# Optimization experiments

Measured on AMD Instinct MI355X. Metric: run time of the kernel, lower is better.

Reference implementation:

```python
import math
import jax, jax.numpy as jnp
import numpy as np

NUM_HEADS = 32

def _alibi_slopes(n: int) -> jnp.ndarray:
    cp2 = 2 ** int(math.floor(math.log2(n)))
    base = 2.0 ** (-(2.0 ** (-(math.log2(cp2) - 3))))
    slopes = base ** np.arange(1, cp2 + 1, dtype=np.float64)
    if cp2 != n:
        extra_base = 2.0 ** (-(2.0 ** (-(math.log2(2 * cp2) - 3))))
        rem = min(cp2, n - cp2)
        slopes = np.concatenate([slopes, extra_base ** np.arange(1, 1 + 2 * rem, 2, dtype=np.float64)])
    return jnp.asarray(slopes, dtype=jnp.float32)


def setup_inputs() -> dict:
    key = jax.random.key(0)
    k1, k2, k3 = jax.random.split(key, 3)
    B, S, E, H, D = 2, 2048, 4096, NUM_HEADS, 128
    hidden_states = jax.random.normal(k1, (B, S, E), dtype=jnp.float32)
    # torch Linear y = x @ W^T; we store transposed weights [in, out]
    w_qkv = jax.random.normal(k2, (E, H * D + 2 * D), dtype=jnp.float32) * 0.02
    w_c = jax.random.normal(k3, (E, E), dtype=jnp.float32) * 0.02
    return {"hidden_states": hidden_states, "w_qkv": w_qkv, "w_c": w_c}


def reference(hidden_states, w_qkv, w_c):
    B, S, E = hidden_states.shape
    H = NUM_HEADS
    D = E // H
    scaling = D ** -0.5

    qkv = hidden_states @ w_qkv                      # [B,S,H*D+2D]
    q = qkv[..., : H * D].reshape(B, S, H, D)        # [B,S,H,D]
    k = qkv[..., H * D: H * D + D]                   # [B,S,D] single KV head (MQA)
    v = qkv[..., H * D + D:]                         # [B,S,D]

    pos = jnp.arange(S)
    slopes = _alibi_slopes(H)                        # [H]
    # ALiBi: slope * (k_pos - q_pos), <= 0 in the causal region
    bias = slopes[:, None, None] * (pos[None, None, :] - pos[None, :, None]).astype(jnp.float32)  # [H,S,S]

    scores = jnp.einsum('bqhd,bkd->bhqk', q, k) * scaling + bias[None]  # [B,H,S,S]
    causal = pos[:, None] >= pos[None, :]            # [S,S]
    scores = jnp.where(causal[None, None], scores, jnp.finfo(scores.dtype).min)
    probs = jax.nn.softmax(scores, axis=-1)
    attn = jnp.einsum('bhqk,bkd->bqhd', probs, v).reshape(B, S, E)
    return attn @ w_c
```

## Files before the change

kernel.cpp:

```cpp
#include <hip/hip_runtime.h>
#include <hip/hip_bf16.h>

typedef unsigned short u16;
typedef unsigned int u32;
typedef __attribute__((ext_vector_type(8))) short s16x8;
typedef __attribute__((ext_vector_type(4))) float f32x4;

#define MFMA_BF16(a, b, c) __builtin_amdgcn_mfma_f32_16x16x32_bf16(a, b, c, 0, 0, 0)

__device__ __forceinline__ u16 f2bf(float f) {
  union { float f; u32 u; } c; c.f = f;
  return (u16)((c.u + 0x7FFFu + ((c.u >> 16) & 1u)) >> 16);
}

__device__ __forceinline__ u32 pkbf(float a, float b) {
  float2 t; t.x = a; t.y = b;
  __hip_bfloat162 h = __float22bfloat162_rn(t);
  union { __hip_bfloat162 h; u32 u; } c; c.h = h; return c.u;
}

__device__ __forceinline__ void gll16(const void* g, void* l) {
  __builtin_amdgcn_global_load_lds((const __attribute__((address_space(1))) void*)g,
                                   (__attribute__((address_space(3))) void*)l, 16, 0, 0);
}

__device__ __forceinline__ f32x4 f4zero() { f32x4 z = {0.f, 0.f, 0.f, 0.f}; return z; }

__global__ void cvt_bf16_kernel(const float4* __restrict__ in, u16* __restrict__ out, int n4) {
  int i = blockIdx.x * 256 + threadIdx.x;
  if (i >= n4) return;
  float4 v = in[i];
  uint2 w;
  w.x = (u32)f2bf(v.x) | ((u32)f2bf(v.y) << 16);
  w.y = (u32)f2bf(v.z) | ((u32)f2bf(v.w) << 16);
  *reinterpret_cast<uint2*>(out + (size_t)i * 4) = w;
}

__global__ void transpose_cvt_kernel(const float* __restrict__ in, u16* __restrict__ out,
                                     int R, int C) {
  __shared__ float tile[32][33];
  int tx = threadIdx.x, ty = threadIdx.y;
  int r0 = blockIdx.y * 32, c0 = blockIdx.x * 32;
#pragma unroll
  for (int i = 0; i < 32; i += 8)
    tile[ty + i][tx] = in[(size_t)(r0 + ty + i) * C + c0 + tx];
  __syncthreads();
#pragma unroll
  for (int i = 0; i < 32; i += 8)
    out[(size_t)(c0 + ty + i) * R + r0 + tx] = f2bf(tile[tx][ty + i]);
}


#define BARRIER __builtin_amdgcn_s_barrier()
#define SCHEDB __builtin_amdgcn_sched_barrier(0)
#define PRIO1 __builtin_amdgcn_s_setprio(1)
#define PRIO0 __builtin_amdgcn_s_setprio(0)
#define VM3 asm volatile("s_waitcnt vmcnt(3)" ::: "memory")
#define VM0 asm volatile("s_waitcnt vmcnt(0)" ::: "memory")
#define NOPW do {} while (0)

#define PAB(P) ((P) * 8192)
#define PBB(P) (24576 + (P) * 16384)

#define RDAB(P) do { _Pragma("unroll")                                                   \
  for (int mi2 = 0; mi2 < 4; ++mi2)                                                      \
    a[mi2] = *(const s16x8*)(smem + PAB(P) + aOff + mi2*1024);                           \
  _Pragma("unroll")                                                                      \
  for (int ni2 = 0; ni2 < 4; ++ni2)                                                      \
    b[ni2] = *(const s16x8*)(smem + PBB(P) + bOff + ni2*1024);                           \
} while (0)

#define MFMA16 do { _Pragma("unroll")                                                    \
  for (int mi2 = 0; mi2 < 4; ++mi2) { _Pragma("unroll")                                  \
    for (int ni2 = 0; ni2 < 4; ++ni2)                                                    \
      acc[mi2][ni2] = MFMA_BF16(a[mi2], b[ni2], acc[mi2][ni2]);                          \
  } } while (0)

#define STAGE3(P, kn) do {                                                               \
  gll16(srcA + (kn), smem + PAB(P) + tt*16);                                             \
  gll16(srcB0 + (kn), smem + PBB(P) + tt*16);                                            \
  gll16(srcB1 + (kn), smem + PBB(P) + 8192 + tt*16);                                     \
} while (0)

#define TILE_S(PR, PS, T) do {                                                           \
  s16x8 a[4], b[4];                                                                      \
  RDAB(PR);                                                                              \
  STAGE3(PS, ((T) + 2) * 32);                                                            \
  SCHEDB;                                                                                \
  PRIO1; MFMA16; PRIO0;                                                                  \
  SCHEDB;                                                                                \
  VM3;                                                                                   \
  BARRIER;                                                                               \
} while (0)

#define TILE_T(PR, WAIT) do {                                                            \
  s16x8 a[4], b[4];                                                                      \
  RDAB(PR);                                                                              \
  SCHEDB;                                                                                \
  PRIO1; MFMA16; PRIO0;                                                                  \
  SCHEDB;                                                                                \
  WAIT;                                                                                  \
  BARRIER;                                                                               \
} while (0)

template<int EPI>
__global__ __launch_bounds__(512, 4)
void gemm128_kernel(const u16* __restrict__ A, const u16* __restrict__ Bt,
                    float* __restrict__ Cf, u16* __restrict__ Cq,
                    u16* __restrict__ Ck, u16* __restrict__ Cvt,
                    int N, int K) {
  __shared__ __align__(16) char smem[73728];
  const int tt = threadIdx.x;
  const int w = tt >> 6, l = tt & 63;
  const int li = l & 15, g = l >> 4;
  const int wm = w >> 2, wn = w & 3;

  const int gx = gridDim.x;
  const int nwg = gx * gridDim.y;
  int id = blockIdx.y * gx + blockIdx.x;
  id = (id & 7) * (nwg >> 3) + (id >> 3);
  const int bn = id % gx, bm = id / gx;

  f32x4 acc[4][4];
#pragma unroll
  for (int i = 0; i < 4; ++i)
#pragma unroll
    for (int j = 0; j < 4; ++j) acc[i][j] = f4zero();

  const int sg = (tt & 7) ^ ((tt >> 3) & 7);
  const int ar = 2 * (tt >> 3) + (sg >> 2);
  const int aq = sg & 3;
  const u16* srcA = A + (size_t)(bm * 128 + ar) * K + aq * 8;
  const u16* srcB0 = Bt + (size_t)(bn * 256 + ar) * K + aq * 8;
  const u16* srcB1 = srcB0 + (size_t)128 * K;

  const int slot = (((li & 1) * 4 + g) ^ ((li >> 1) & 7)) * 16;
  const int aOff = wm * 4096 + (li >> 1) * 128 + slot;
  const int bOff = wn * 4096 + (li >> 1) * 128 + slot;

  STAGE3(0, 0);
  STAGE3(1, 32);
  VM3;
  BARRIER;

  for (int t3 = 0; t3 < 126; t3 += 3) {
    TILE_S(0, 2, t3);
    TILE_S(1, 0, t3 + 1);
    TILE_S(2, 1, t3 + 2);
  }
  TILE_T(0, VM0);
  TILE_T(1, NOPW);

#pragma unroll
  for (int mi = 0; mi < 4; ++mi) {
#pragma unroll
    for (int ni = 0; ni < 4; ++ni) {
      const int row0 = bm * 128 + wm * 64 + mi * 16 + g * 4;
      const int col = bn * 256 + wn * 64 + ni * 16 + li;
#pragma unroll
      for (int r = 0; r < 4; ++r) {
        const int m = row0 + r;
        const float v = acc[mi][ni][r];
        if (EPI == 0) {
          Cf[(size_t)m * N + col] = v;
        } else {
          const int bb2 = m >> 11, s = m & 2047;
          const int kt = s >> 5;
          const size_t tb = (size_t)(bb2 * 64 + kt);
          if (col < 4096) {
            Cq[(size_t)m * 4096 + col] = f2bf(v);
          } else if (col < 4224) {
            const int d = col - 4096, kr = s & 31;
            const int mk = kr >> 4, lii = kr & 15;
            const int kk = d >> 5, gg = (d >> 3) & 3, e = d & 7;
            Ck[(tb * 8 + mk * 4 + kk) * 512 + (gg * 16 + lii) * 8 + e] = f2bf(v);
          } else {
            const int d = col - 4224, kp = s & 31;
            const int mf = d >> 4, lii = d & 15;
            const int gg = kp >> 3, e = kp & 7;
            Cvt[(tb * 8 + mf) * 512 + (gg * 16 + lii) * 8 + e] = f2bf(v);
          }
        }
      }
    }
  }
}


__device__ __forceinline__ void load_ktile(s16x8 (&dst)[8], const u16* kf, size_t tb, int l) {
#pragma unroll
  for (int f = 0; f < 8; ++f)
    dst[f] = *(const s16x8*)&kf[(tb * 8 + f) * 512 + l * 8];
}

template<bool DIAG>
__device__ __forceinline__ void attn_tile(
    int kt, const u16* kf, const u16* vf, size_t bb64, int l, int li, int g,
    s16x8 (&use)[8], s16x8 (&fill)[8], bool do_fill,
    const s16x8 (&bq)[2][4], f32x4 (&acc)[8][2],
    float (&m_)[2], float (&lp)[2], float (&bias)[2],
    float c1, const float (&cjr)[8], float bstep, u16 (*Pw)[40]) {
  const size_t tb = bb64 + kt;
  s16x8 vr[8];
#pragma unroll
  for (int f = 0; f < 8; ++f)
    vr[f] = *(const s16x8*)&vf[(tb * 8 + f) * 512 + l * 8];
  if (do_fill) load_ktile(fill, kf, tb - 1, l);

  f32x4 sc[2][2];
  sc[0][0] = f4zero(); sc[0][1] = f4zero(); sc[1][0] = f4zero(); sc[1][1] = f4zero();
#pragma unroll
  for (int kk = 0; kk < 4; ++kk)
#pragma unroll
    for (int mk = 0; mk < 2; ++mk) {
      sc[mk][0] = MFMA_BF16(use[mk * 4 + kk], bq[0][kk], sc[mk][0]);
      sc[mk][1] = MFMA_BF16(use[mk * 4 + kk], bq[1][kk], sc[mk][1]);
    }

#pragma unroll
  for (int nq = 0; nq < 2; ++nq) {
    float sv[8];
    float pm = -3e38f;
    if (DIAG) {
#pragma unroll
      for (int mk = 0; mk < 2; ++mk)
#pragma unroll
        for (int r = 0; r < 4; ++r) {
          const int kd = mk * 16 + g * 4 + r - (nq * 16 + li);
          float s = fmaf(sc[mk][nq][r], c1, bias[nq] + cjr[mk * 4 + r]);
          s = (kd <= 0) ? s : -1e30f;
          sv[mk * 4 + r] = s;
          pm = fmaxf(pm, s);
        }
      pm = fmaxf(pm, __shfl_xor(pm, 16));
      pm = fmaxf(pm, __shfl_xor(pm, 32));
      m_[nq] = pm;
    } else {
#pragma unroll
      for (int mk = 0; mk < 2; ++mk)
#pragma unroll
        for (int r = 0; r < 4; ++r) {
          float s = fmaf(sc[mk][nq][r], c1, bias[nq] + cjr[mk * 4 + r]);
          sv[mk * 4 + r] = s;
          pm = fmaxf(pm, s);
        }
      if (__any(pm > m_[nq])) {
        pm = fmaxf(pm, __shfl_xor(pm, 16));
        pm = fmaxf(pm, __shfl_xor(pm, 32));
        const float nm = fmaxf(m_[nq], pm);
        const float scale = exp2f(m_[nq] - nm);
#pragma unroll
        for (int mf = 0; mf < 8; ++mf) acc[mf][nq] *= scale;
        lp[nq] *= scale;
        m_[nq] = nm;
      }
    }
    const float mref = m_[nq];
    float e[8];
#pragma unroll
    for (int j = 0; j < 8; ++j) e[j] = exp2f(sv[j] - mref);
    lp[nq] += ((e[0] + e[1]) + (e[2] + e[3])) + ((e[4] + e[5]) + (e[6] + e[7]));
#pragma unroll
    for (int mk = 0; mk < 2; ++mk) {
      uint2 wv;
      wv.x = pkbf(e[mk * 4 + 0], e[mk * 4 + 1]);
      wv.y = pkbf(e[mk * 4 + 2], e[mk * 4 + 3]);
      *reinterpret_cast<uint2*>(&Pw[nq * 16 + li][mk * 16 + g * 4]) = wv;
    }
    bias[nq] -= bstep;
  }

  s16x8 pb0 = *(const s16x8*)&Pw[li][g * 8];
  s16x8 pb1 = *(const s16x8*)&Pw[16 + li][g * 8];
#pragma unroll
  for (int mf = 0; mf < 8; ++mf) {
    acc[mf][0] = MFMA_BF16(vr[mf], pb0, acc[mf][0]);
    acc[mf][1] = MFMA_BF16(vr[mf], pb1, acc[mf][1]);
  }
}

__device__ __forceinline__ void attn_qtile(
    int qt, int h, int b, const u16* qbuf, const u16* kf, const u16* vf,
    u16* obuf, int l, int li, int g, float c1, float sl2, u16 (*Pw)[40]) {
  const int S = 2048;
  const int q0 = qt * 32;
  const size_t bb64 = (size_t)b * 64;

  s16x8 bq[2][4];
#pragma unroll
  for (int nq = 0; nq < 2; ++nq)
#pragma unroll
    for (int kk = 0; kk < 4; ++kk)
      bq[nq][kk] = *(const s16x8*)&qbuf[(size_t)(b * S + q0 + nq * 16 + li) * 4096
                                        + h * 128 + kk * 32 + g * 8];

  f32x4 acc[8][2];
#pragma unroll
  for (int mf = 0; mf < 8; ++mf) { acc[mf][0] = f4zero(); acc[mf][1] = f4zero(); }
  float m_[2] = {-3e38f, -3e38f};
  float lp[2] = {0.f, 0.f};

  float cjr[8];
#pragma unroll
  for (int j = 0; j < 8; ++j) cjr[j] = sl2 * (float)((j >> 2) * 16 + (j & 3));
  float bias[2];
#pragma unroll
  for (int nq = 0; nq < 2; ++nq)
    bias[nq] = sl2 * (float)(g * 4 - nq * 16 - li);
  const float bstep = sl2 * 32.f;

  s16x8 kA[8], kB[8];
  load_ktile(kA, kf, bb64 + qt, l);
  attn_tile<true>(qt, kf, vf, bb64, l, li, g, kA, kB, qt >= 1,
                  bq, acc, m_, lp, bias, c1, cjr, bstep, Pw);
  int kt = qt - 1;
  while (kt >= 1) {
    attn_tile<false>(kt, kf, vf, bb64, l, li, g, kB, kA, true,
                     bq, acc, m_, lp, bias, c1, cjr, bstep, Pw);
    attn_tile<false>(kt - 1, kf, vf, bb64, l, li, g, kA, kB, kt >= 2,
                     bq, acc, m_, lp, bias, c1, cjr, bstep, Pw);
    kt -= 2;
  }
  if (kt == 0)
    attn_tile<false>(0, kf, vf, bb64, l, li, g, kB, kA, false,
                     bq, acc, m_, lp, bias, c1, cjr, bstep, Pw);

#pragma unroll
  for (int nq = 0; nq < 2; ++nq) {
    float ls = lp[nq];
    ls += __shfl_xor(ls, 16);
    ls += __shfl_xor(ls, 32);
    const float inv = 1.f / ls;
    const size_t rowbase = (size_t)(b * S + q0 + nq * 16 + li) * 4096 + h * 128;
#pragma unroll
    for (int mf = 0; mf < 8; ++mf) {
      f32x4 v = acc[mf][nq];
      uint2 wv;
      wv.x = pkbf(v[0] * inv, v[1] * inv);
      wv.y = pkbf(v[2] * inv, v[3] * inv);
      *reinterpret_cast<uint2*>(&obuf[rowbase + mf * 16 + g * 4]) = wv;
    }
  }
}

__global__ __launch_bounds__(64, 2)
void attn_kernel(const u16* __restrict__ qbuf, const u16* __restrict__ kf,
                 const u16* __restrict__ vf, u16* __restrict__ obuf) {
  const int p = blockIdx.x, h = blockIdx.y, b = blockIdx.z;
  const int l = threadIdx.x, li = l & 15, g = l >> 4;
  const float L2E = 1.4426950408889634f;
  const float slope = exp2f(-0.25f * (float)(h + 1));
  const float c1 = 0.08838834764831845f * L2E;
  const float sl2 = slope * L2E;
  __shared__ __align__(16) u16 P[32][40];
  attn_qtile(63 - p, h, b, qbuf, kf, vf, obuf, l, li, g, c1, sl2, P);
  attn_qtile(p, h, b, qbuf, kf, vf, obuf, l, li, g, c1, sl2, P);
}

extern "C" void kernel_launch(void* const* d_in, const int* in_sizes, int n_in,
                              void* d_out, int out_size, void* d_ws, size_t ws_size,
                              hipStream_t stream) {
  (void)in_sizes; (void)n_in; (void)out_size; (void)ws_size;
  const float* hidden = (const float*)d_in[0];
  const float* w_qkv = (const float*)d_in[1];
  const float* w_c = (const float*)d_in[2];
  float* out = (float*)d_out;
  char* ws = (char*)d_ws;

  u16* hid_bf = (u16*)(ws + 0);
  u16* wT     = (u16*)(ws + 33554432);
  u16* qbuf   = (u16*)(ws + 69206016);
  u16* kbuf   = (u16*)(ws + 102760448);
  u16* vtbuf  = (u16*)(ws + 103809024);

  cvt_bf16_kernel<<<16384, 256, 0, stream>>>((const float4*)hidden, hid_bf, 4194304);
  transpose_cvt_kernel<<<dim3(136, 128), dim3(32, 8), 0, stream>>>(w_qkv, wT, 4096, 4352);
  gemm128_kernel<1><<<dim3(17, 32), 512, 0, stream>>>(hid_bf, wT, nullptr, qbuf, kbuf, vtbuf,
                                                      4352, 4096);
  attn_kernel<<<dim3(32, 32, 2), 64, 0, stream>>>(qbuf, kbuf, vtbuf, hid_bf);
  transpose_cvt_kernel<<<dim3(128, 128), dim3(32, 8), 0, stream>>>(w_c, wT, 4096, 4096);
  gemm128_kernel<0><<<dim3(16, 32), 512, 0, stream>>>(hid_bf, wT, out, nullptr, nullptr, nullptr,
                                                      4096, 4096);
}
```

Before: 486.3 us.

## Pre-swizzle weights into MFMA fragment layout and load B directly to registers

```diff
diff --git a/kernel.cpp b/kernel.cpp
--- a/kernel.cpp
+++ b/kernel.cpp
@@ -36,8 +36,8 @@
   *reinterpret_cast<uint2*>(out + (size_t)i * 4) = w;
 }
 
-__global__ void transpose_cvt_kernel(const float* __restrict__ in, u16* __restrict__ out,
-                                     int R, int C) {
+__global__ void transpose_cvt_frag_kernel(const float* __restrict__ in, u16* __restrict__ out,
+                                          int R, int C) {
   __shared__ float tile[32][33];
   int tx = threadIdx.x, ty = threadIdx.y;
   int r0 = blockIdx.y * 32, c0 = blockIdx.x * 32;
@@ -45,9 +45,15 @@
   for (int i = 0; i < 32; i += 8)
     tile[ty + i][tx] = in[(size_t)(r0 + ty + i) * C + c0 + tx];
   __syncthreads();
-#pragma unroll
-  for (int i = 0; i < 32; i += 8)
-    out[(size_t)(c0 + ty + i) * R + r0 + tx] = f2bf(tile[tx][ty + i]);
+  const int KT = R >> 5;
+  const int kt = r0 >> 5;
+  const int q = tx >> 3, e = tx & 7;
+#pragma unroll
+  for (int i = 0; i < 32; i += 8) {
+    const int n = c0 + ty + i;
+    const int nb = n >> 4, li2 = n & 15;
+    out[((size_t)nb * KT + kt) * 512 + (q * 16 + li2) * 8 + e] = f2bf(tile[tx][ty + i]);
+  }
 }
 
 
@@ -55,19 +61,20 @@
 #define SCHEDB __builtin_amdgcn_sched_barrier(0)
 #define PRIO1 __builtin_amdgcn_s_setprio(1)
 #define PRIO0 __builtin_amdgcn_s_setprio(0)
-#define VM3 asm volatile("s_waitcnt vmcnt(3)" ::: "memory")
+#define VM1 asm volatile("s_waitcnt vmcnt(1)" ::: "memory")
 #define VM0 asm volatile("s_waitcnt vmcnt(0)" ::: "memory")
 #define NOPW do {} while (0)
 
 #define PAB(P) ((P) * 8192)
-#define PBB(P) (24576 + (P) * 16384)
-
-#define RDAB(P) do { _Pragma("unroll")                                                   \
+
+#define RDA(P) do { _Pragma("unroll")                                                    \
   for (int mi2 = 0; mi2 < 4; ++mi2)                                                      \
     a[mi2] = *(const s16x8*)(smem + PAB(P) + aOff + mi2*1024);                           \
-  _Pragma("unroll")                                                                      \
+} while (0)
+
+#define LDB(T) do { _Pragma("unroll")                                                    \
   for (int ni2 = 0; ni2 < 4; ++ni2)                                                      \
-    b[ni2] = *(const s16x8*)(smem + PBB(P) + bOff + ni2*1024);                           \
+    b[ni2] = *(const s16x8*)(Bw + ((size_t)ni2 * 128 + (T)) * 512);                      \
 } while (0)
 
 #define MFMA16 do { _Pragma("unroll")                                                    \
@@ -76,26 +83,24 @@
       acc[mi2][ni2] = MFMA_BF16(a[mi2], b[ni2], acc[mi2][ni2]);                          \
   } } while (0)
 
-#define STAGE3(P, kn) do {                                                               \
-  gll16(srcA + (kn), smem + PAB(P) + tt*16);                                             \
-  gll16(srcB0 + (kn), smem + PBB(P) + tt*16);                                            \
-  gll16(srcB1 + (kn), smem + PBB(P) + 8192 + tt*16);                                     \
-} while (0)
+#define STAGE1(P, kn) gll16(srcA + (kn), smem + PAB(P) + tt*16)
 
 #define TILE_S(PR, PS, T) do {                                                           \
   s16x8 a[4], b[4];                                                                      \
-  RDAB(PR);                                                                              \
-  STAGE3(PS, ((T) + 2) * 32);                                                            \
+  LDB(T);                                                                                \
+  RDA(PR);                                                                               \
+  STAGE1(PS, ((T) + 2) * 32);                                                            \
   SCHEDB;                                                                                \
   PRIO1; MFMA16; PRIO0;                                                                  \
   SCHEDB;                                                                                \
-  VM3;                                                                                   \
+  VM1;                                                                                   \
   BARRIER;                                                                               \
 } while (0)
 
-#define TILE_T(PR, WAIT) do {                                                            \
+#define TILE_T(PR, T, WAIT) do {                                                         \
   s16x8 a[4], b[4];                                                                      \
-  RDAB(PR);                                                                              \
+  LDB(T);                                                                                \
+  RDA(PR);                                                                               \
   SCHEDB;                                                                                \
   PRIO1; MFMA16; PRIO0;                                                                  \
   SCHEDB;                                                                                \
@@ -105,11 +110,11 @@
 
 template<int EPI>
 __global__ __launch_bounds__(512, 4)
-void gemm128_kernel(const u16* __restrict__ A, const u16* __restrict__ Bt,
+void gemm128_kernel(const u16* __restrict__ A, const u16* __restrict__ Bf,
                     float* __restrict__ Cf, u16* __restrict__ Cq,
                     u16* __restrict__ Ck, u16* __restrict__ Cvt,
-                    int N, int K) {
-  __shared__ __align__(16) char smem[73728];
+                    int N) {
+  __shared__ __align__(16) char smem[24576];
   const int tt = threadIdx.x;
   const int w = tt >> 6, l = tt & 63;
   const int li = l & 15, g = l >> 4;
@@ -130,17 +135,16 @@
   const int sg = (tt & 7) ^ ((tt >> 3) & 7);
   const int ar = 2 * (tt >> 3) + (sg >> 2);
   const int aq = sg & 3;
-  const u16* srcA = A + (size_t)(bm * 128 + ar) * K + aq * 8;
-  const u16* srcB0 = Bt + (size_t)(bn * 256 + ar) * K + aq * 8;
-  const u16* srcB1 = srcB0 + (size_t)128 * K;
+  const u16* srcA = A + (size_t)(bm * 128 + ar) * 4096 + aq * 8;
+
+  const u16* Bw = Bf + ((size_t)(bn * 16 + wn * 4) * 128) * 512 + l * 8;
 
   const int slot = (((li & 1) * 4 + g) ^ ((li >> 1) & 7)) * 16;
   const int aOff = wm * 4096 + (li >> 1) * 128 + slot;
-  const int bOff = wn * 4096 + (li >> 1) * 128 + slot;
-
-  STAGE3(0, 0);
-  STAGE3(1, 32);
-  VM3;
+
+  STAGE1(0, 0);
+  STAGE1(1, 32);
+  VM1;
   BARRIER;
 
   for (int t3 = 0; t3 < 126; t3 += 3) {
@@ -148,8 +152,8 @@
     TILE_S(1, 0, t3 + 1);
     TILE_S(2, 1, t3 + 2);
   }
-  TILE_T(0, VM0);
-  TILE_T(1, NOPW);
+  TILE_T(0, 126, VM0);
+  TILE_T(1, 127, NOPW);
 
 #pragma unroll
   for (int mi = 0; mi < 4; ++mi) {
@@ -374,11 +378,11 @@
   u16* vtbuf  = (u16*)(ws + 103809024);
 
   cvt_bf16_kernel<<<16384, 256, 0, stream>>>((const float4*)hidden, hid_bf, 4194304);
-  transpose_cvt_kernel<<<dim3(136, 128), dim3(32, 8), 0, stream>>>(w_qkv, wT, 4096, 4352);
+  transpose_cvt_frag_kernel<<<dim3(136, 128), dim3(32, 8), 0, stream>>>(w_qkv, wT, 4096, 4352);
   gemm128_kernel<1><<<dim3(17, 32), 512, 0, stream>>>(hid_bf, wT, nullptr, qbuf, kbuf, vtbuf,
-                                                      4352, 4096);
+                                                      4352);
   attn_kernel<<<dim3(32, 32, 2), 64, 0, stream>>>(qbuf, kbuf, vtbuf, hid_bf);
-  transpose_cvt_kernel<<<dim3(128, 128), dim3(32, 8), 0, stream>>>(w_c, wT, 4096, 4096);
+  transpose_cvt_frag_kernel<<<dim3(128, 128), dim3(32, 8), 0, stream>>>(w_c, wT, 4096, 4096);
   gemm128_kernel<0><<<dim3(16, 32), 512, 0, stream>>>(hid_bf, wT, out, nullptr, nullptr, nullptr,
-                                                      4096, 4096);
-}
+                                                      4096);
+}
```

New measurement: 502.6 us. 1.03x slower.
